# Performance work log

Measured on AMD Instinct MI355X. Metric: run time of the kernel, lower is better.

The kernel has to match this reference:

```python
import jax, jax.numpy as jnp
import numpy as np

N_NODES = 100000
N_EDGES = 1600000
D_IN = 128
D_OUT = 128


def setup_inputs() -> dict:
    key = jax.random.key(0)
    k_x, k_r, k_c, k_v, k_w = jax.random.split(key, 5)
    X = jax.random.normal(k_x, (N_NODES, D_IN), dtype=jnp.float32)
    A_rows = jax.random.randint(k_r, (N_EDGES,), 0, N_NODES, dtype=jnp.int32)
    A_cols = jax.random.randint(k_c, (N_EDGES,), 0, N_NODES, dtype=jnp.int32)
    A_vals = jax.random.uniform(k_v, (N_EDGES,), dtype=jnp.float32)
    # Xavier-uniform linear weight [out, in], zero bias (matches reset_parameters)
    limit = float(np.sqrt(6.0 / (D_IN + D_OUT)))
    W = jax.random.uniform(k_w, (D_OUT, D_IN), dtype=jnp.float32, minval=-limit, maxval=limit)
    b = jnp.zeros((D_OUT,), dtype=jnp.float32)
    return {"X": X, "A_rows": A_rows, "A_cols": A_cols, "A_vals": A_vals, "W": W, "b": b}


def reference(X, A_rows, A_cols, A_vals, W, b):
    # h = A_sparse @ X  (COO SpMM: gather neighbor features, scale, scatter-add by row)
    msgs = A_vals[:, None] * X[A_cols]          # [E, D_IN]
    h = jax.ops.segment_sum(msgs, A_rows, num_segments=N_NODES)  # [N, D_IN]
    # dense linear projection
    return h @ W.T + b
```

## Files before the change

### kernel.cpp

```cpp
#include <hip/hip_runtime.h>

#define N_NODES_C 100000
#define N_EDGES_C 1600000
#define D_C 128
#define NBKT 1563
#define RPB 64
#define CAP 1536
#define PTILE 4096
#define NPB ((N_EDGES_C + PTILE - 1) / PTILE)
#define WB_STRIDE 136

static __device__ __forceinline__ unsigned short f2bf(float x) {
    unsigned u = __float_as_uint(x);
    unsigned r = 0x7fffu + ((u >> 16) & 1u);
    return (unsigned short)((u + r) >> 16);
}
static __device__ __forceinline__ float bflo(unsigned u) { return __uint_as_float(u << 16); }
static __device__ __forceinline__ float bfhi(unsigned u) { return __uint_as_float(u & 0xffff0000u); }

typedef __attribute__((ext_vector_type(8))) __bf16 bf16x8;
typedef __attribute__((ext_vector_type(4))) float f32x4;
union FragU { uint4 u; bf16x8 b; };

__global__ __launch_bounds__(256) void gemm_mfma(const float* __restrict__ X,
                                                 const float* __restrict__ W,
                                                 unsigned short* __restrict__ Y, int n) {
    __shared__ unsigned short Wb[128 * WB_STRIDE];

    const int tid = threadIdx.x;
    const int wave = tid >> 6;
    const int lane = tid & 63;
    const int m16 = lane & 15;
    const int quad = lane >> 4;

    const int row0 = blockIdx.x * 64 + wave * 16;
    int row = row0 + m16;
    int rowc = (row < n) ? row : (n - 1);

    float4 xv[4][2];
    const float* xp = X + (long)rowc * D_C + quad * 8;
#pragma unroll
    for (int s = 0; s < 4; ++s) {
        xv[s][0] = *(const float4*)(xp + s * 32);
        xv[s][1] = *(const float4*)(xp + s * 32 + 4);
    }

    for (int i = tid; i < 128 * 32; i += 256) {
        int o = i >> 5;
        int k4 = (i & 31) * 4;
        float4 w = *(const float4*)&W[o * 128 + k4];
        uint2 p;
        p.x = (unsigned)f2bf(w.x) | ((unsigned)f2bf(w.y) << 16);
        p.y = (unsigned)f2bf(w.z) | ((unsigned)f2bf(w.w) << 16);
        *(uint2*)&Wb[o * WB_STRIDE + k4] = p;
    }
    __syncthreads();

    FragU a[4];
#pragma unroll
    for (int s = 0; s < 4; ++s) {
        a[s].u.x = (unsigned)f2bf(xv[s][0].x) | ((unsigned)f2bf(xv[s][0].y) << 16);
        a[s].u.y = (unsigned)f2bf(xv[s][0].z) | ((unsigned)f2bf(xv[s][0].w) << 16);
        a[s].u.z = (unsigned)f2bf(xv[s][1].x) | ((unsigned)f2bf(xv[s][1].y) << 16);
        a[s].u.w = (unsigned)f2bf(xv[s][1].z) | ((unsigned)f2bf(xv[s][1].w) << 16);
    }

    f32x4 acc[8];
#pragma unroll
    for (int t = 0; t < 8; ++t) acc[t] = (f32x4){0.f, 0.f, 0.f, 0.f};

#pragma unroll
    for (int s = 0; s < 4; ++s) {
#pragma unroll
        for (int t = 0; t < 8; ++t) {
            FragU bf;
            bf.u = *(const uint4*)&Wb[(t * 16 + m16) * WB_STRIDE + s * 32 + quad * 8];
            acc[t] = __builtin_amdgcn_mfma_f32_16x16x32_bf16(a[s].b, bf.b, acc[t], 0, 0, 0);
        }
    }

#pragma unroll
    for (int t = 0; t < 8; ++t) {
#pragma unroll
        for (int r = 0; r < 4; ++r) {
            int orow = row0 + quad * 4 + r;
            if (orow < n) Y[(long)orow * D_C + t * 16 + m16] = f2bf(acc[t][r]);
        }
    }
}

__global__ __launch_bounds__(256) void partition(const int* __restrict__ rows,
                                                 const int* __restrict__ cols,
                                                 const float* __restrict__ vals,
                                                 int* __restrict__ gcount,
                                                 int2* __restrict__ staging, int E) {
    __shared__ int lhist[NBKT];
    __shared__ int lbase[NBKT];
    __shared__ unsigned short ebkt[PTILE];
    __shared__ unsigned short ernk[PTILE];
    const int tid = threadIdx.x;
    const int t0 = blockIdx.x * PTILE;

    for (int i = tid; i < NBKT; i += 256) lhist[i] = 0;
    __syncthreads();

#pragma unroll
    for (int k = 0; k < PTILE / 256; ++k) {
        int e = t0 + k * 256 + tid;
        if (e < E) {
            int bkt = rows[e] >> 6;
            int rnk = atomicAdd(&lhist[bkt], 1);
            ebkt[k * 256 + tid] = (unsigned short)bkt;
            ernk[k * 256 + tid] = (unsigned short)rnk;
        }
    }
    __syncthreads();

    for (int i = tid; i < NBKT; i += 256)
        lbase[i] = lhist[i] ? atomicAdd(&gcount[i], lhist[i]) : 0;
    __syncthreads();

#pragma unroll
    for (int k = 0; k < PTILE / 256; ++k) {
        int e = t0 + k * 256 + tid;
        if (e < E) {
            int li = k * 256 + tid;
            int bkt = ebkt[li];
            int dst = lbase[bkt] + ernk[li];
            if (dst < CAP) {
                int rl = rows[e] & (RPB - 1);
                int2 p;
                p.x = cols[e] | (rl << 17);
                p.y = __float_as_int(vals[e]);
                staging[(long)bkt * CAP + dst] = p;
            }
        }
    }
}

__global__ __launch_bounds__(256) void sort_aggregate(const int* __restrict__ gcount,
                                                      const int2* __restrict__ staging,
                                                      const unsigned short* __restrict__ Y,
                                                      const float* __restrict__ bias,
                                                      float* __restrict__ out, int n) {
    __shared__ int2 pl[CAP];
    __shared__ int hist[RPB];
    __shared__ int lcur[RPB];
    __shared__ int rbegL[RPB];
    __shared__ int rcntL[RPB];

    const int bb = blockIdx.x, tid = threadIdx.x;
    int cnt = gcount[bb];
    if (cnt > CAP) cnt = CAP;
    const long s = (long)bb * CAP;

    if (tid < RPB) hist[tid] = 0;
    __syncthreads();

    for (int i = tid; i < cnt; i += 256) {
        int rl = ((unsigned)staging[s + i].x) >> 17;
        atomicAdd(&hist[rl], 1);
    }
    __syncthreads();

    int v = (tid < RPB) ? hist[tid] : 0;
    for (int off = 1; off < RPB; off <<= 1) {
        int t = (tid >= off && tid < RPB) ? hist[tid - off] : 0;
        __syncthreads();
        if (tid < RPB) hist[tid] += t;
        __syncthreads();
    }
    if (tid < RPB) {
        int excl = hist[tid] - v;
        lcur[tid] = excl;
        rbegL[tid] = excl;
        rcntL[tid] = v;
    }
    __syncthreads();

    for (int i = tid; i < cnt; i += 256) {
        int2 p = staging[s + i];
        int rl = ((unsigned)p.x) >> 17;
        int slot = atomicAdd(&lcur[rl], 1);
        pl[slot] = p;
    }
    __syncthreads();

    const int lane = tid & 15;
    const unsigned short* Yl = Y + lane * 8;
    float4 b0 = *(const float4*)&bias[lane * 8];
    float4 b1 = *(const float4*)&bias[lane * 8 + 4];

#pragma unroll
    for (int pass = 0; pass < RPB / 16; ++pass) {
        int rlocal = pass * 16 + (tid >> 4);
        int row = bb * RPB + rlocal;
        if (row >= n) continue;

        int i = rbegL[rlocal];
        int e = i + rcntL[rlocal];

        float acc[8];
        acc[0] = b0.x; acc[1] = b0.y; acc[2] = b0.z; acc[3] = b0.w;
        acc[4] = b1.x; acc[5] = b1.y; acc[6] = b1.z; acc[7] = b1.w;

        for (; i + 8 <= e; i += 8) {
            int2 p[8];
            uint4 y[8];
#pragma unroll
            for (int u = 0; u < 8; ++u) p[u] = pl[i + u];
#pragma unroll
            for (int u = 0; u < 8; ++u)
                y[u] = *(const uint4*)&Yl[(long)(p[u].x & 0x1FFFF) * D_C];
#pragma unroll
            for (int u = 0; u < 8; ++u) {
                float v2 = __int_as_float(p[u].y);
                acc[0] += v2 * bflo(y[u].x); acc[1] += v2 * bfhi(y[u].x);
                acc[2] += v2 * bflo(y[u].y); acc[3] += v2 * bfhi(y[u].y);
                acc[4] += v2 * bflo(y[u].z); acc[5] += v2 * bfhi(y[u].z);
                acc[6] += v2 * bflo(y[u].w); acc[7] += v2 * bfhi(y[u].w);
            }
        }
        for (; i + 4 <= e; i += 4) {
            int2 p[4];
            uint4 y[4];
#pragma unroll
            for (int u = 0; u < 4; ++u) p[u] = pl[i + u];
#pragma unroll
            for (int u = 0; u < 4; ++u)
                y[u] = *(const uint4*)&Yl[(long)(p[u].x & 0x1FFFF) * D_C];
#pragma unroll
            for (int u = 0; u < 4; ++u) {
                float v2 = __int_as_float(p[u].y);
                acc[0] += v2 * bflo(y[u].x); acc[1] += v2 * bfhi(y[u].x);
                acc[2] += v2 * bflo(y[u].y); acc[3] += v2 * bfhi(y[u].y);
                acc[4] += v2 * bflo(y[u].z); acc[5] += v2 * bfhi(y[u].z);
                acc[6] += v2 * bflo(y[u].w); acc[7] += v2 * bfhi(y[u].w);
            }
        }
        for (; i < e; ++i) {
            int2 p = pl[i];
            uint4 y = *(const uint4*)&Yl[(long)(p.x & 0x1FFFF) * D_C];
            float v2 = __int_as_float(p.y);
            acc[0] += v2 * bflo(y.x); acc[1] += v2 * bfhi(y.x);
            acc[2] += v2 * bflo(y.y); acc[3] += v2 * bfhi(y.y);
            acc[4] += v2 * bflo(y.z); acc[5] += v2 * bfhi(y.z);
            acc[6] += v2 * bflo(y.w); acc[7] += v2 * bfhi(y.w);
        }

        f32x4 o0 = {acc[0], acc[1], acc[2], acc[3]};
        f32x4 o1 = {acc[4], acc[5], acc[6], acc[7]};
        f32x4* op = (f32x4*)&out[(long)row * D_C + lane * 8];
        __builtin_nontemporal_store(o0, op);
        __builtin_nontemporal_store(o1, op + 1);
    }
}

__global__ __launch_bounds__(256) void init_out(const float* __restrict__ b,
                                                float* __restrict__ out, int n) {
    int idx = blockIdx.x * 256 + threadIdx.x;
    int total = n * (D_C / 4);
    if (idx < total) {
        int o4 = idx & (D_C / 4 - 1);
        ((float4*)out)[idx] = ((const float4*)b)[o4];
    }
}

__global__ __launch_bounds__(256) void scatter_edges(const int* __restrict__ rows,
                                                     const int* __restrict__ cols,
                                                     const float* __restrict__ vals,
                                                     const unsigned short* __restrict__ Y,
                                                     float* __restrict__ out, int E) {
    int e = blockIdx.x * 8 + (threadIdx.x >> 5);
    if (e >= E) return;
    int lane = threadIdx.x & 31;
    int row = rows[e];
    int col = cols[e];
    float v = vals[e];
    uint2 y = *(const uint2*)&Y[(long)col * D_C + lane * 4];
    float* dst = out + (long)row * D_C + lane * 4;
    unsafeAtomicAdd(dst + 0, v * bflo(y.x));
    unsafeAtomicAdd(dst + 1, v * bfhi(y.x));
    unsafeAtomicAdd(dst + 2, v * bflo(y.y));
    unsafeAtomicAdd(dst + 3, v * bfhi(y.y));
}

extern "C" void kernel_launch(void* const* d_in, const int* in_sizes, int n_in,
                              void* d_out, int out_size, void* d_ws, size_t ws_size,
                              hipStream_t stream) {
    const float* X  = (const float*)d_in[0];
    const int*   Ar = (const int*)d_in[1];
    const int*   Ac = (const int*)d_in[2];
    const float* Av = (const float*)d_in[3];
    const float* W  = (const float*)d_in[4];
    const float* b  = (const float*)d_in[5];
    float* out = (float*)d_out;

    unsigned short* Y = (unsigned short*)d_ws;
    int2* staging = (int2*)(Y + 12800000);
    int* gcount   = (int*)(staging + (size_t)NBKT * CAP);
    size_t need = (size_t)12800000 * 2 + (size_t)NBKT * CAP * 8 + (size_t)NBKT * 4;

    gemm_mfma<<<(N_NODES_C + 63) / 64, 256, 0, stream>>>(X, W, Y, N_NODES_C);

    if (ws_size >= need) {
        (void)hipMemsetAsync(gcount, 0, NBKT * sizeof(int), stream);
        partition<<<NPB, 256, 0, stream>>>(Ar, Ac, Av, gcount, staging, N_EDGES_C);
        sort_aggregate<<<NBKT, 256, 0, stream>>>(gcount, staging, Y, b, out, N_NODES_C);
    } else {
        init_out<<<(N_NODES_C * (D_C / 4) + 255) / 256, 256, 0, stream>>>(b, out, N_NODES_C);
        scatter_edges<<<(N_EDGES_C + 7) / 8, 256, 0, stream>>>(Ar, Ac, Av, Y, out, N_EDGES_C);
    }
}
```

Measured before the change: 242.1 us.

## Fuse edge partition with GEMM blocks and split aggregation blocks by row halves

```diff
diff --git a/kernel.cpp b/kernel.cpp
--- a/kernel.cpp
+++ b/kernel.cpp
@@ -6,8 +6,10 @@
 #define NBKT 1563
 #define RPB 64
 #define CAP 1536
+#define CAP_H 768
 #define PTILE 4096
 #define NPB ((N_EDGES_C + PTILE - 1) / PTILE)
+#define NGB ((N_NODES_C + 63) / 64)
 #define WB_STRIDE 136
 
 static __device__ __forceinline__ unsigned short f2bf(float x) {
@@ -21,6 +23,268 @@
 typedef __attribute__((ext_vector_type(8))) __bf16 bf16x8;
 typedef __attribute__((ext_vector_type(4))) float f32x4;
 union FragU { uint4 u; bf16x8 b; };
+
+__global__ __launch_bounds__(256) void prep(const float* __restrict__ W,
+                                            unsigned short* __restrict__ Wbf,
+                                            int* __restrict__ gcount) {
+    int t = blockIdx.x * 256 + threadIdx.x;
+    if (t < 4096) {
+        float4 w = ((const float4*)W)[t];
+        uint2 p;
+        p.x = (unsigned)f2bf(w.x) | ((unsigned)f2bf(w.y) << 16);
+        p.y = (unsigned)f2bf(w.z) | ((unsigned)f2bf(w.w) << 16);
+        ((uint2*)Wbf)[t] = p;
+    } else {
+        int j = t - 4096;
+        if (j < NBKT) gcount[j] = 0;
+    }
+}
+
+union SMemF {
+    struct {
+        int lhist[NBKT];
+        int lbase[NBKT];
+        unsigned short ebkt[PTILE];
+        unsigned short ernk[PTILE];
+    } part;
+    unsigned short ytile[4][16 * WB_STRIDE];
+};
+
+__global__ __launch_bounds__(256) void fused(const float* __restrict__ X,
+                                             const int* __restrict__ rows,
+                                             const int* __restrict__ cols,
+                                             const float* __restrict__ vals,
+                                             const unsigned short* __restrict__ Wbf,
+                                             int* __restrict__ gcount,
+                                             int2* __restrict__ staging,
+                                             unsigned short* __restrict__ Y,
+                                             int n, int E) {
+    __shared__ SMemF sm;
+    const int tid = threadIdx.x;
+
+    if (blockIdx.x < NPB) {
+        const int t0 = blockIdx.x * PTILE;
+
+        for (int i = tid; i < NBKT; i += 256) sm.part.lhist[i] = 0;
+        __syncthreads();
+
+#pragma unroll
+        for (int k = 0; k < PTILE / 256; ++k) {
+            int e = t0 + k * 256 + tid;
+            if (e < E) {
+                int bkt = rows[e] >> 6;
+                int rnk = atomicAdd(&sm.part.lhist[bkt], 1);
+                sm.part.ebkt[k * 256 + tid] = (unsigned short)bkt;
+                sm.part.ernk[k * 256 + tid] = (unsigned short)rnk;
+            }
+        }
+        __syncthreads();
+
+        for (int i = tid; i < NBKT; i += 256)
+            sm.part.lbase[i] = sm.part.lhist[i] ? atomicAdd(&gcount[i], sm.part.lhist[i]) : 0;
+        __syncthreads();
+
+#pragma unroll
+        for (int k = 0; k < PTILE / 256; ++k) {
+            int e = t0 + k * 256 + tid;
+            if (e < E) {
+                int li = k * 256 + tid;
+                int bkt = sm.part.ebkt[li];
+                int dst = sm.part.lbase[bkt] + sm.part.ernk[li];
+                if (dst < CAP) {
+                    int rl = rows[e] & (RPB - 1);
+                    int2 p;
+                    p.x = cols[e] | (rl << 17);
+                    p.y = __float_as_int(vals[e]);
+                    staging[(long)bkt * CAP + dst] = p;
+                }
+            }
+        }
+        return;
+    }
+
+    const int g = blockIdx.x - NPB;
+    const int wave = tid >> 6;
+    const int lane = tid & 63;
+    const int m16 = lane & 15;
+    const int quad = lane >> 4;
+
+    const int row0 = g * 64 + wave * 16;
+    int row = row0 + m16;
+    int rowc = (row < n) ? row : (n - 1);
+
+    FragU a[4];
+    const float* xp = X + (long)rowc * D_C + quad * 8;
+#pragma unroll
+    for (int s = 0; s < 4; ++s) {
+        float4 x0 = *(const float4*)(xp + s * 32);
+        float4 x1 = *(const float4*)(xp + s * 32 + 4);
+        a[s].u.x = (unsigned)f2bf(x0.x) | ((unsigned)f2bf(x0.y) << 16);
+        a[s].u.y = (unsigned)f2bf(x0.z) | ((unsigned)f2bf(x0.w) << 16);
+        a[s].u.z = (unsigned)f2bf(x1.x) | ((unsigned)f2bf(x1.y) << 16);
+        a[s].u.w = (unsigned)f2bf(x1.z) | ((unsigned)f2bf(x1.w) << 16);
+    }
+
+    f32x4 acc[8];
+#pragma unroll
+    for (int t = 0; t < 8; ++t) acc[t] = (f32x4){0.f, 0.f, 0.f, 0.f};
+
+#pragma unroll
+    for (int s = 0; s < 4; ++s) {
+#pragma unroll
+        for (int t = 0; t < 8; ++t) {
+            FragU bf;
+            bf.u = *(const uint4*)&Wbf[(t * 16 + m16) * D_C + s * 32 + quad * 8];
+            acc[t] = __builtin_amdgcn_mfma_f32_16x16x32_bf16(a[s].b, bf.b, acc[t], 0, 0, 0);
+        }
+    }
+
+    unsigned short* yt = sm.ytile[wave];
+#pragma unroll
+    for (int t = 0; t < 8; ++t)
+#pragma unroll
+        for (int r = 0; r < 4; ++r)
+            yt[(quad * 4 + r) * WB_STRIDE + t * 16 + m16] = f2bf(acc[t][r]);
+    __syncthreads();
+
+#pragma unroll
+    for (int h = 0; h < 2; ++h) {
+        int row_l = h * 8 + (lane >> 3);
+        int orow = row0 + row_l;
+        if (orow < n) {
+            const unsigned short* src = &yt[row_l * WB_STRIDE + (lane & 7) * 16];
+            uint4 v0 = *(const uint4*)(src);
+            uint4 v1 = *(const uint4*)(src + 8);
+            uint4* dst = (uint4*)&Y[(long)orow * D_C + (lane & 7) * 16];
+            dst[0] = v0;
+            dst[1] = v1;
+        }
+    }
+}
+
+__global__ __launch_bounds__(256) void sort_aggregate(const int* __restrict__ gcount,
+                                                      const int2* __restrict__ staging,
+                                                      const unsigned short* __restrict__ Y,
+                                                      const float* __restrict__ bias,
+                                                      float* __restrict__ out, int n) {
+    __shared__ int2 pl[CAP_H];
+    __shared__ int hist[32];
+    __shared__ int lcur[32];
+    __shared__ int rbegL[32];
+    __shared__ int rcntL[32];
+
+    const int bb = blockIdx.x >> 1;
+    const int half = blockIdx.x & 1;
+    const int tid = threadIdx.x;
+    int cnt = gcount[bb];
+    if (cnt > CAP) cnt = CAP;
+    const long s = (long)bb * CAP;
+
+    if (tid < 32) hist[tid] = 0;
+    __syncthreads();
+
+    const unsigned* sx = (const unsigned*)(staging + s);
+    for (int i = tid; i < cnt; i += 256) {
+        int rl = sx[2 * i] >> 17;
+        if ((rl >> 5) == half) atomicAdd(&hist[rl & 31], 1);
+    }
+    __syncthreads();
+
+    int v = (tid < 32) ? hist[tid] : 0;
+    for (int off = 1; off < 32; off <<= 1) {
+        int t = (tid >= off && tid < 32) ? hist[tid - off] : 0;
+        __syncthreads();
+        if (tid < 32) hist[tid] += t;
+        __syncthreads();
+    }
+    if (tid < 32) {
+        int excl = hist[tid] - v;
+        lcur[tid] = excl;
+        rbegL[tid] = excl;
+        rcntL[tid] = v;
+    }
+    __syncthreads();
+
+    for (int i = tid; i < cnt; i += 256) {
+        int2 p = staging[s + i];
+        int rl = ((unsigned)p.x) >> 17;
+        if ((rl >> 5) == half) {
+            int slot = atomicAdd(&lcur[rl & 31], 1);
+            if (slot < CAP_H) pl[slot] = p;
+        }
+    }
+    __syncthreads();
+
+    const int lane = tid & 15;
+    const unsigned short* Yl = Y + lane * 8;
+    float4 b0 = *(const float4*)&bias[lane * 8];
+    float4 b1 = *(const float4*)&bias[lane * 8 + 4];
+
+#pragma unroll
+    for (int pass = 0; pass < 2; ++pass) {
+        int rlocal = pass * 16 + (tid >> 4);
+        int row = bb * RPB + half * 32 + rlocal;
+        if (row >= n) continue;
+
+        int i = rbegL[rlocal];
+        int e = i + rcntL[rlocal];
+        if (e > CAP_H) e = CAP_H;
+
+        float acc[8];
+        acc[0] = b0.x; acc[1] = b0.y; acc[2] = b0.z; acc[3] = b0.w;
+        acc[4] = b1.x; acc[5] = b1.y; acc[6] = b1.z; acc[7] = b1.w;
+
+        for (; i + 8 <= e; i += 8) {
+            int2 p[8];
+            uint4 y[8];
+#pragma unroll
+            for (int u = 0; u < 8; ++u) p[u] = pl[i + u];
+#pragma unroll
+            for (int u = 0; u < 8; ++u)
+                y[u] = *(const uint4*)&Yl[(long)(p[u].x & 0x1FFFF) * D_C];
+#pragma unroll
+            for (int u = 0; u < 8; ++u) {
+                float v2 = __int_as_float(p[u].y);
+                acc[0] += v2 * bflo(y[u].x); acc[1] += v2 * bfhi(y[u].x);
+                acc[2] += v2 * bflo(y[u].y); acc[3] += v2 * bfhi(y[u].y);
+                acc[4] += v2 * bflo(y[u].z); acc[5] += v2 * bfhi(y[u].z);
+                acc[6] += v2 * bflo(y[u].w); acc[7] += v2 * bfhi(y[u].w);
+            }
+        }
+        for (; i + 4 <= e; i += 4) {
+            int2 p[4];
+            uint4 y[4];
+#pragma unroll
+            for (int u = 0; u < 4; ++u) p[u] = pl[i + u];
+#pragma unroll
+            for (int u = 0; u < 4; ++u)
+                y[u] = *(const uint4*)&Yl[(long)(p[u].x & 0x1FFFF) * D_C];
+#pragma unroll
+            for (int u = 0; u < 4; ++u) {
+                float v2 = __int_as_float(p[u].y);
+                acc[0] += v2 * bflo(y[u].x); acc[1] += v2 * bfhi(y[u].x);
+                acc[2] += v2 * bflo(y[u].y); acc[3] += v2 * bfhi(y[u].y);
+                acc[4] += v2 * bflo(y[u].z); acc[5] += v2 * bfhi(y[u].z);
+                acc[6] += v2 * bflo(y[u].w); acc[7] += v2 * bfhi(y[u].w);
+            }
+        }
+        for (; i < e; ++i) {
+            int2 p = pl[i];
+            uint4 y = *(const uint4*)&Yl[(long)(p.x & 0x1FFFF) * D_C];
+            float v2 = __int_as_float(p.y);
+            acc[0] += v2 * bflo(y.x); acc[1] += v2 * bfhi(y.x);
+            acc[2] += v2 * bflo(y.y); acc[3] += v2 * bfhi(y.y);
+            acc[4] += v2 * bflo(y.z); acc[5] += v2 * bfhi(y.z);
+            acc[6] += v2 * bflo(y.w); acc[7] += v2 * bfhi(y.w);
+        }
+
+        f32x4 o0 = {acc[0], acc[1], acc[2], acc[3]};
+        f32x4 o1 = {acc[4], acc[5], acc[6], acc[7]};
+        f32x4* op = (f32x4*)&out[(long)row * D_C + lane * 8];
+        __builtin_nontemporal_store(o0, op);
+        __builtin_nontemporal_store(o1, op + 1);
+    }
+}
 
 __global__ __launch_bounds__(256) void gemm_mfma(const float* __restrict__ X,
                                                  const float* __restrict__ W,
@@ -86,173 +350,6 @@
             int orow = row0 + quad * 4 + r;
             if (orow < n) Y[(long)orow * D_C + t * 16 + m16] = f2bf(acc[t][r]);
         }
-    }
-}
-
-__global__ __launch_bounds__(256) void partition(const int* __restrict__ rows,
-                                                 const int* __restrict__ cols,
-                                                 const float* __restrict__ vals,
-                                                 int* __restrict__ gcount,
-                                                 int2* __restrict__ staging, int E) {
-    __shared__ int lhist[NBKT];
-    __shared__ int lbase[NBKT];
-    __shared__ unsigned short ebkt[PTILE];
-    __shared__ unsigned short ernk[PTILE];
-    const int tid = threadIdx.x;
-    const int t0 = blockIdx.x * PTILE;
-
-    for (int i = tid; i < NBKT; i += 256) lhist[i] = 0;
-    __syncthreads();
-
-#pragma unroll
-    for (int k = 0; k < PTILE / 256; ++k) {
-        int e = t0 + k * 256 + tid;
-        if (e < E) {
-            int bkt = rows[e] >> 6;
-            int rnk = atomicAdd(&lhist[bkt], 1);
-            ebkt[k * 256 + tid] = (unsigned short)bkt;
-            ernk[k * 256 + tid] = (unsigned short)rnk;
-        }
-    }
-    __syncthreads();
-
-    for (int i = tid; i < NBKT; i += 256)
-        lbase[i] = lhist[i] ? atomicAdd(&gcount[i], lhist[i]) : 0;
-    __syncthreads();
-
-#pragma unroll
-    for (int k = 0; k < PTILE / 256; ++k) {
-        int e = t0 + k * 256 + tid;
-        if (e < E) {
-            int li = k * 256 + tid;
-            int bkt = ebkt[li];
-            int dst = lbase[bkt] + ernk[li];
-            if (dst < CAP) {
-                int rl = rows[e] & (RPB - 1);
-                int2 p;
-                p.x = cols[e] | (rl << 17);
-                p.y = __float_as_int(vals[e]);
-                staging[(long)bkt * CAP + dst] = p;
-            }
-        }
-    }
-}
-
-__global__ __launch_bounds__(256) void sort_aggregate(const int* __restrict__ gcount,
-                                                      const int2* __restrict__ staging,
-                                                      const unsigned short* __restrict__ Y,
-                                                      const float* __restrict__ bias,
-                                                      float* __restrict__ out, int n) {
-    __shared__ int2 pl[CAP];
-    __shared__ int hist[RPB];
-    __shared__ int lcur[RPB];
-    __shared__ int rbegL[RPB];
-    __shared__ int rcntL[RPB];
-
-    const int bb = blockIdx.x, tid = threadIdx.x;
-    int cnt = gcount[bb];
-    if (cnt > CAP) cnt = CAP;
-    const long s = (long)bb * CAP;
-
-    if (tid < RPB) hist[tid] = 0;
-    __syncthreads();
-
-    for (int i = tid; i < cnt; i += 256) {
-        int rl = ((unsigned)staging[s + i].x) >> 17;
-        atomicAdd(&hist[rl], 1);
-    }
-    __syncthreads();
-
-    int v = (tid < RPB) ? hist[tid] : 0;
-    for (int off = 1; off < RPB; off <<= 1) {
-        int t = (tid >= off && tid < RPB) ? hist[tid - off] : 0;
-        __syncthreads();
-        if (tid < RPB) hist[tid] += t;
-        __syncthreads();
-    }
-    if (tid < RPB) {
-        int excl = hist[tid] - v;
-        lcur[tid] = excl;
-        rbegL[tid] = excl;
-        rcntL[tid] = v;
-    }
-    __syncthreads();
-
-    for (int i = tid; i < cnt; i += 256) {
-        int2 p = staging[s + i];
-        int rl = ((unsigned)p.x) >> 17;
-        int slot = atomicAdd(&lcur[rl], 1);
-        pl[slot] = p;
-    }
-    __syncthreads();
-
-    const int lane = tid & 15;
-    const unsigned short* Yl = Y + lane * 8;
-    float4 b0 = *(const float4*)&bias[lane * 8];
-    float4 b1 = *(const float4*)&bias[lane * 8 + 4];
-
-#pragma unroll
-    for (int pass = 0; pass < RPB / 16; ++pass) {
-        int rlocal = pass * 16 + (tid >> 4);
-        int row = bb * RPB + rlocal;
-        if (row >= n) continue;
-
-        int i = rbegL[rlocal];
-        int e = i + rcntL[rlocal];
-
-        float acc[8];
-        acc[0] = b0.x; acc[1] = b0.y; acc[2] = b0.z; acc[3] = b0.w;
-        acc[4] = b1.x; acc[5] = b1.y; acc[6] = b1.z; acc[7] = b1.w;
-
-        for (; i + 8 <= e; i += 8) {
-            int2 p[8];
-            uint4 y[8];
-#pragma unroll
-            for (int u = 0; u < 8; ++u) p[u] = pl[i + u];
-#pragma unroll
-            for (int u = 0; u < 8; ++u)
-                y[u] = *(const uint4*)&Yl[(long)(p[u].x & 0x1FFFF) * D_C];
-#pragma unroll
-            for (int u = 0; u < 8; ++u) {
-                float v2 = __int_as_float(p[u].y);
-                acc[0] += v2 * bflo(y[u].x); acc[1] += v2 * bfhi(y[u].x);
-                acc[2] += v2 * bflo(y[u].y); acc[3] += v2 * bfhi(y[u].y);
-                acc[4] += v2 * bflo(y[u].z); acc[5] += v2 * bfhi(y[u].z);
-                acc[6] += v2 * bflo(y[u].w); acc[7] += v2 * bfhi(y[u].w);
-            }
-        }
-        for (; i + 4 <= e; i += 4) {
-            int2 p[4];
-            uint4 y[4];
-#pragma unroll
-            for (int u = 0; u < 4; ++u) p[u] = pl[i + u];
-#pragma unroll
-            for (int u = 0; u < 4; ++u)
-                y[u] = *(const uint4*)&Yl[(long)(p[u].x & 0x1FFFF) * D_C];
-#pragma unroll
-            for (int u = 0; u < 4; ++u) {
-                float v2 = __int_as_float(p[u].y);
-                acc[0] += v2 * bflo(y[u].x); acc[1] += v2 * bfhi(y[u].x);
-                acc[2] += v2 * bflo(y[u].y); acc[3] += v2 * bfhi(y[u].y);
-                acc[4] += v2 * bflo(y[u].z); acc[5] += v2 * bfhi(y[u].z);
-                acc[6] += v2 * bflo(y[u].w); acc[7] += v2 * bfhi(y[u].w);
-            }
-        }
-        for (; i < e; ++i) {
-            int2 p = pl[i];
-            uint4 y = *(const uint4*)&Yl[(long)(p.x & 0x1FFFF) * D_C];
-            float v2 = __int_as_float(p.y);
-            acc[0] += v2 * bflo(y.x); acc[1] += v2 * bfhi(y.x);
-            acc[2] += v2 * bflo(y.y); acc[3] += v2 * bfhi(y.y);
-            acc[4] += v2 * bflo(y.z); acc[5] += v2 * bfhi(y.z);
-            acc[6] += v2 * bflo(y.w); acc[7] += v2 * bfhi(y.w);
-        }
-
-        f32x4 o0 = {acc[0], acc[1], acc[2], acc[3]};
-        f32x4 o1 = {acc[4], acc[5], acc[6], acc[7]};
-        f32x4* op = (f32x4*)&out[(long)row * D_C + lane * 8];
-        __builtin_nontemporal_store(o0, op);
-        __builtin_nontemporal_store(o1, op + 1);
     }
 }
 
@@ -298,16 +395,17 @@
 
     unsigned short* Y = (unsigned short*)d_ws;
     int2* staging = (int2*)(Y + 12800000);
-    int* gcount   = (int*)(staging + (size_t)NBKT * CAP);
-    size_t need = (size_t)12800000 * 2 + (size_t)NBKT * CAP * 8 + (size_t)NBKT * 4;
-
-    gemm_mfma<<<(N_NODES_C + 63) / 64, 256, 0, stream>>>(X, W, Y, N_NODES_C);
+    unsigned short* Wbf = (unsigned short*)(staging + (size_t)NBKT * CAP);
+    int* gcount = (int*)(Wbf + 16384);
+    size_t need = (size_t)12800000 * 2 + (size_t)NBKT * CAP * 8 + 32768 + (size_t)NBKT * 4;
 
     if (ws_size >= need) {
-        (void)hipMemsetAsync(gcount, 0, NBKT * sizeof(int), stream);
-        partition<<<NPB, 256, 0, stream>>>(Ar, Ac, Av, gcount, staging, N_EDGES_C);
-        sort_aggregate<<<NBKT, 256, 0, stream>>>(gcount, staging, Y, b, out, N_NODES_C);
+        prep<<<23, 256, 0, stream>>>(W, Wbf, gcount);
+        fused<<<NPB + NGB, 256, 0, stream>>>(X, Ar, Ac, Av, Wbf, gcount, staging, Y,
+                                             N_NODES_C, N_EDGES_C);
+        sort_aggregate<<<2 * NBKT, 256, 0, stream>>>(gcount, staging, Y, b, out, N_NODES_C);
     } else {
+        gemm_mfma<<<(N_NODES_C + 63) / 64, 256, 0, stream>>>(X, W, Y, N_NODES_C);
         init_out<<<(N_NODES_C * (D_C / 4) + 255) / 256, 256, 0, stream>>>(b, out, N_NODES_C);
         scatter_edges<<<(N_EDGES_C + 7) / 8, 256, 0, stream>>>(Ar, Ac, Av, Y, out, N_EDGES_C);
     }
```

Result: no change. 242.0 us (-0.0%).
